# Performance work log

Hardware: AMD Instinct MI355X
Metric: run time of the kernel (lower is better)

Reference implementation:

```python
import jax, jax.numpy as jnp
import numpy as np

B, S, D, H = 2, 2048, 1024, 16
HD = D // H  # head dim 64
LN_EPS = 1e-12


def setup_inputs() -> dict:
    key = jax.random.key(0)
    ks = jax.random.split(key, 10)
    sc = 0.02
    return {
        "input_tensor": jax.random.normal(ks[0], (B, S, D), dtype=jnp.float32),
        "attention_mask": jnp.zeros((B, 1, 1, S), dtype=jnp.float32),
        "Wq": jax.random.normal(ks[1], (D, D), dtype=jnp.float32) * sc,
        "bq": jnp.zeros((D,), dtype=jnp.float32),
        "Wk": jax.random.normal(ks[2], (D, D), dtype=jnp.float32) * sc,
        "bk": jnp.zeros((D,), dtype=jnp.float32),
        "Wv": jax.random.normal(ks[3], (D, D), dtype=jnp.float32) * sc,
        "bv": jnp.zeros((D,), dtype=jnp.float32),
        "Wo": jax.random.normal(ks[4], (D, D), dtype=jnp.float32) * sc,
        "bo": jnp.zeros((D,), dtype=jnp.float32),
        "ln_gamma": jnp.ones((D,), dtype=jnp.float32),
        "ln_beta": jnp.zeros((D,), dtype=jnp.float32),
    }


def _split_heads(x):
    # [B,S,D] -> [B,H,S,hd]
    return x.reshape(B, S, H, HD).transpose(0, 2, 1, 3)


def reference(input_tensor, attention_mask, Wq, bq, Wk, bk, Wv, bv, Wo, bo, ln_gamma, ln_beta):
    q = _split_heads(input_tensor @ Wq + bq)
    k = _split_heads(input_tensor @ Wk + bk)
    v = _split_heads(input_tensor @ Wv + bv)
    scores = jnp.einsum("bhqd,bhkd->bhqk", q, k) / jnp.sqrt(jnp.float32(HD))
    scores = scores + attention_mask  # additive mask broadcast
    probs = jax.nn.softmax(scores, axis=-1)
    ctx = jnp.einsum("bhqk,bhkd->bhqd", probs, v)
    ctx = ctx.transpose(0, 2, 1, 3).reshape(B, S, D)
    hidden = ctx @ Wo + bo
    x = hidden + input_tensor
    mu = jnp.mean(x, axis=-1, keepdims=True)
    var = jnp.mean(jnp.square(x - mu), axis=-1, keepdims=True)
    return (x - mu) / jnp.sqrt(var + LN_EPS) * ln_gamma + ln_beta
```

## Files before the change

### kernel.cpp

```cpp
#include <hip/hip_runtime.h>
#include <stdint.h>

#define Bb 2
#define Ss 2048
#define Dd 1024
#define Hh 16
#define HD 64
#define Mtot 4096

typedef __bf16 bf16x8 __attribute__((ext_vector_type(8)));
typedef float f32x4 __attribute__((ext_vector_type(4)));
typedef float f32x16 __attribute__((ext_vector_type(16)));
typedef unsigned short ushort_t;

#if __has_builtin(__builtin_amdgcn_exp2f)
#define EXP2(x) __builtin_amdgcn_exp2f(x)
#else
#define EXP2(x) __expf((x) * 0.6931472f)
#endif

__device__ __forceinline__ float bf2f(ushort_t u) {
    union { uint32_t i; float f; } v;
    v.i = ((uint32_t)u) << 16;
    return v.f;
}

__device__ __forceinline__ ushort_t f2bf(float f) {
    union { float f; uint32_t i; } v;
    v.f = f;
    uint32_t u = v.i;
    u += 0x7FFFu + ((u >> 16) & 1u);
    return (ushort_t)(u >> 16);
}

__device__ __forceinline__ uint32_t cvtpk_bf16(float lo, float hi) {
    uint32_t r;
    asm("v_cvt_pk_bf16_f32 %0, %1, %2" : "=v"(r) : "v"(lo), "v"(hi));
    return r;
}

__device__ __forceinline__ float load_in(const void* p, size_t i, int isf32) {
    if (isf32) return ((const float*)p)[i];
    return bf2f(((const ushort_t*)p)[i]);
}

__device__ __forceinline__ void gload_lds16(const void* g, void* l) {
    __builtin_amdgcn_global_load_lds(
        (const __attribute__((address_space(1))) void*)g,
        (__attribute__((address_space(3))) void*)l, 16, 0, 0);
}

#define NVEC 525568ull
__global__ __launch_bounds__(256) void prep_k(
    const void* X, const void* mask, const void* bq, const void* bk,
    const void* bv, const void* bo, const void* g, const void* be,
    const void* Wq, const void* Wk, const void* Wv, const void* Wo,
    int* __restrict__ flag, ushort_t* __restrict__ cX,
    ushort_t* __restrict__ cMask, ushort_t* __restrict__ cB,
    ushort_t* __restrict__ wt) {
    __shared__ int sflag;
    __shared__ ushort_t tile[32][33];
    const int tid = threadIdx.x;
    {
        const int lane = tid & 63;
        if (tid < 64) {
            const ushort_t* Xu = (const ushort_t*)X;
            int local = 0;
            for (int i = lane; i < 2048; i += 64) {
                int e = (Xu[i] >> 7) & 0xFF;
                local += (e >= 0x90);
            }
            for (int off = 1; off < 64; off <<= 1) local += __shfl_xor(local, off);
            if (lane == 0) sflag = (local >= 4) ? 1 : 0;
        }
    }
    __syncthreads();
    const int f = sflag;
    if (blockIdx.x == 0 && tid == 0) *flag = f;

    if (blockIdx.x < 1024) {
        const size_t stride = 1024ull * 256ull;
        for (size_t t = (size_t)blockIdx.x * 256 + tid; t < NVEC; t += stride) {
            const void* src;
            ushort_t* dst;
            size_t v;
            if (t < 524288ull) {
                src = X; dst = cX; v = t;
            } else if (t < 524800ull) {
                src = mask; dst = cMask; v = t - 524288ull;
            } else {
                size_t j = t - 524800ull;
                int w = (int)(j >> 7);
                src = (w == 0) ? bq : (w == 1) ? bk : (w == 2) ? bv
                    : (w == 3) ? bo : (w == 4) ? g : be;
                dst = cB + w * 1024;
                v = j & 127;
            }
            if (f) {
                const float4* s4 = (const float4*)src;
                float4 a = s4[v * 2], b = s4[v * 2 + 1];
                union { ushort_t u[8]; uint4 q; } pk;
                pk.u[0] = f2bf(a.x); pk.u[1] = f2bf(a.y);
                pk.u[2] = f2bf(a.z); pk.u[3] = f2bf(a.w);
                pk.u[4] = f2bf(b.x); pk.u[5] = f2bf(b.y);
                pk.u[6] = f2bf(b.z); pk.u[7] = f2bf(b.w);
                ((uint4*)dst)[v] = pk.q;
            } else {
                ((uint4*)dst)[v] = ((const uint4*)src)[v];
            }
        }
    } else {
        int id2 = blockIdx.x - 1024;
        int z = id2 >> 10;
        int rem = id2 & 1023;
        int bx = rem & 31, by = rem >> 5;
        const void* W = (z == 0) ? Wq : (z == 1) ? Wk : (z == 2) ? Wv : Wo;
        ushort_t* T = wt + (size_t)z * Dd * Dd;
        int tx = tid & 31, ty = tid >> 5;
        int x = bx * 32 + tx;
        int y0 = by * 32;
        for (int i = 0; i < 4; i++) {
            int y = y0 + ty + i * 8;
            tile[ty + i * 8][tx] = f2bf(load_in(W, (size_t)y * Dd + x, f));
        }
        __syncthreads();
        int x2 = by * 32 + tx;
        int y20 = bx * 32;
        for (int i = 0; i < 4; i++) {
            int y = y20 + ty + i * 8;
            T[(size_t)y * Dd + x2] = tile[tx][ty + i * 8];
        }
    }
}

__global__ __launch_bounds__(256) void gemm_qkv(
    const ushort_t* __restrict__ X, const ushort_t* __restrict__ wt,
    const ushort_t* __restrict__ cB,
    ushort_t* __restrict__ Qb, ushort_t* __restrict__ Kb, ushort_t* __restrict__ Vtb) {
    const int z = blockIdx.z;
    const ushort_t* Wt = wt + (size_t)z * Dd * Dd;
    const ushort_t* bias = cB + z * 1024;

    __shared__ __align__(16) ushort_t smem[2][2][128 * 32];

    const int tid = threadIdx.x;
    const int lane = tid & 63, wv = tid >> 6;
    const int quad = lane >> 4, l15 = lane & 15;
    const int wrow = (wv >> 1) * 64, wcol = (wv & 1) * 64;
    const int row0 = blockIdx.y * 128, col0 = blockIdx.x * 128;
    const int lrow = lane >> 2, lcol = (lane & 3) * 8;

    const f32x4 fzero = {0.f, 0.f, 0.f, 0.f};
    f32x4 acc[4][4];
    for (int mt = 0; mt < 4; mt++)
        for (int nt = 0; nt < 4; nt++) acc[mt][nt] = fzero;

    for (int j = 0; j < 2; j++) {
        int ch = wv * 2 + j;
        gload_lds16(&X[(size_t)(row0 + ch * 16 + lrow) * Dd + lcol],
                    &smem[0][0][ch * 512]);
        gload_lds16(&Wt[(size_t)(col0 + ch * 16 + lrow) * Dd + lcol],
                    &smem[0][1][ch * 512]);
    }

    for (int k0 = 0; k0 < Dd; k0 += 32) {
        const int buf = (k0 >> 5) & 1;
        __syncthreads();
        if (k0 + 32 < Dd) {
            for (int j = 0; j < 2; j++) {
                int ch = wv * 2 + j;
                gload_lds16(&X[(size_t)(row0 + ch * 16 + lrow) * Dd + k0 + 32 + lcol],
                            &smem[buf ^ 1][0][ch * 512]);
                gload_lds16(&Wt[(size_t)(col0 + ch * 16 + lrow) * Dd + k0 + 32 + lcol],
                            &smem[buf ^ 1][1][ch * 512]);
            }
        }
        const ushort_t* As = &smem[buf][0][0];
        const ushort_t* Bs = &smem[buf][1][0];
        bf16x8 af[4], bfr[4];
        for (int mt = 0; mt < 4; mt++)
            af[mt] = *(const bf16x8*)(&As[(wrow + mt * 16 + l15) * 32 + quad * 8]);
        for (int nt = 0; nt < 4; nt++)
            bfr[nt] = *(const bf16x8*)(&Bs[(wcol + nt * 16 + l15) * 32 + quad * 8]);
        for (int mt = 0; mt < 4; mt++)
            for (int nt = 0; nt < 4; nt++)
                acc[mt][nt] = __builtin_amdgcn_mfma_f32_16x16x32_bf16(
                    af[mt], bfr[nt], acc[mt][nt], 0, 0, 0);
    }

    const float qscale = 0.18033688f;
    ushort_t* Cs = &smem[0][0][0];
    for (int mt = 0; mt < 4; mt++) {
        __syncthreads();
        for (int nt = 0; nt < 4; nt++) {
            int gn = col0 + wcol + nt * 16 + l15;
            float bv_ = bf2f(bias[gn]);
            for (int r = 0; r < 4; r++) {
                float v = acc[mt][nt][r] + bv_;
                if (z == 0) v *= qscale;
                int ric = (wv >> 1) * 16 + quad * 4 + r;
                Cs[ric * 136 + wcol + nt * 16 + l15] = f2bf(v);
            }
        }
        __syncthreads();
        if (z == 2) {
            int c = tid >> 1, r0 = (tid & 1) * 16;
            int gn = col0 + c, h = gn >> 6, d = gn & 63;
            int gmbase = row0 + (r0 >> 4) * 64 + mt * 16;
            int b = gmbase >> 11, s0 = gmbase & 2047;
            union { ushort_t u[16]; uint4 q[2]; } pk;
            for (int i = 0; i < 16; i++) pk.u[i] = Cs[(r0 + i) * 136 + c];
            uint4* dst = (uint4*)&Vtb[((size_t)((b * Hh + h) * HD + d)) * Ss + s0];
            dst[0] = pk.q[0];
            dst[1] = pk.q[1];
        } else {
            int ric = tid >> 3, c0 = (tid & 7) * 16;
            int gm = row0 + (ric >> 4) * 64 + mt * 16 + (ric & 15);
            int gn = col0 + c0, h = gn >> 6, d0 = gn & 63;
            int b = gm >> 11, s = gm & 2047;
            const uint4* src = (const uint4*)&Cs[ric * 136 + c0];
            ushort_t* Ob = (z == 0) ? Qb : Kb;
            uint4* dst = (uint4*)&Ob[((size_t)((b * Hh + h) * Ss + s)) * HD + d0];
            dst[0] = src[0];
            dst[1] = src[1];
        }
    }
}

__global__ __launch_bounds__(512, 4) void attn(
    const ushort_t* __restrict__ Q, const ushort_t* __restrict__ K,
    const ushort_t* __restrict__ Vt, const ushort_t* __restrict__ mask,
    ushort_t* __restrict__ ctx) {
    const int tid = threadIdx.x;
    const int lane = tid & 63, wv = tid >> 6;
    const int wg = wv & 3, g = wv >> 2;
    const int n = lane & 31, hi = lane >> 5;
    const int bh = blockIdx.x;
    const int b = bh >> 4, h = bh & 15;
    const int q0 = blockIdx.y * 128 + wg * 32;
    const int kg = g * 1024;

    const ushort_t* Qh = Q + (size_t)bh * Ss * HD;
    const ushort_t* Kh = K + (size_t)bh * Ss * HD;
    const ushort_t* Vh = Vt + (size_t)bh * HD * Ss;

    __shared__ __align__(16) ushort_t KV[2][2][2][64 * 64];
    __shared__ __align__(16) float maskF[Ss];

    for (int i = tid; i < Ss; i += 512)
        maskF[i] = (bf2f(mask[b * Ss + i]) - 4.0f) * 1.4426950f;

    const int r8 = lane >> 3, c8 = lane & 7, gc = c8 ^ r8;
    const int sw = n & 7;

    for (int j = 0; j < 2; j++) {
        int row = wg * 16 + j * 8;
        gload_lds16(&Kh[(size_t)(kg + row + r8) * HD + gc * 8], &KV[g][0][0][row * 64]);
        gload_lds16(&Vh[(size_t)(row + r8) * Ss + kg + gc * 8], &KV[g][1][0][row * 64]);
    }

    bf16x8 qf[4];
#pragma unroll
    for (int ks = 0; ks < 4; ks++)
        qf[ks] = *(const bf16x8*)(&Qh[(size_t)(q0 + n) * HD + ks * 16 + hi * 8]);

    bf16x8 onesf;
    {
        union { ushort_t u[8]; bf16x8 v; } ou;
        for (int i = 0; i < 8; i++) ou.u[i] = 0x3F80;
        onesf = ou.v;
    }

    f32x16 o[2], o_l;
#pragma unroll
    for (int r = 0; r < 16; r++) { o[0][r] = 0.f; o[1][r] = 0.f; o_l[r] = 0.f; }

    for (int it = 0; it < 16; it++) {
        const int kb = kg + it * 64;
        const int buf = it & 1;
        __syncthreads();

        if (it + 1 < 16) {
            for (int j = 0; j < 2; j++) {
                int row = wg * 16 + j * 8;
                gload_lds16(&Kh[(size_t)(kb + 64 + row + r8) * HD + gc * 8],
                            &KV[g][0][buf ^ 1][row * 64]);
                gload_lds16(&Vh[(size_t)(row + r8) * Ss + kb + 64 + gc * 8],
                            &KV[g][1][buf ^ 1][row * 64]);
            }
        }

        const ushort_t* ks_ = &KV[g][0][buf][0];
        const ushort_t* vs_ = &KV[g][1][buf][0];

        f32x16 st[2];
#pragma unroll
        for (int mt = 0; mt < 2; mt++) {
#pragma unroll
            for (int r4 = 0; r4 < 4; r4++) {
                f32x4 mk = *(const f32x4*)(&maskF[kb + mt * 32 + r4 * 8 + hi * 4]);
                st[mt][r4 * 4 + 0] = mk[0];
                st[mt][r4 * 4 + 1] = mk[1];
                st[mt][r4 * 4 + 2] = mk[2];
                st[mt][r4 * 4 + 3] = mk[3];
            }
        }
        __builtin_amdgcn_s_setprio(1);
#pragma unroll
        for (int mt = 0; mt < 2; mt++) {
#pragma unroll
            for (int ksp = 0; ksp < 4; ksp++) {
                bf16x8 kf = *(const bf16x8*)(
                    &ks_[(mt * 32 + n) * 64 + ((ksp * 2 + hi) ^ sw) * 8]);
                st[mt] = __builtin_amdgcn_mfma_f32_32x32x16_bf16(
                    kf, qf[ksp], st[mt], 0, 0, 0);
            }
        }
        __builtin_amdgcn_s_setprio(0);

#pragma unroll
        for (int mt = 0; mt < 2; mt++)
#pragma unroll
            for (int r = 0; r < 16; r++) st[mt][r] = EXP2(st[mt][r]);

#pragma unroll
        for (int c = 0; c < 4; c++) {
            const int mt = c >> 1, cc = (c & 1) * 8;
            uint32_t a0 = cvtpk_bf16(st[mt][cc + 0], st[mt][cc + 1]);
            uint32_t a1 = cvtpk_bf16(st[mt][cc + 2], st[mt][cc + 3]);
            uint32_t b0 = cvtpk_bf16(st[mt][cc + 4], st[mt][cc + 5]);
            uint32_t b1 = cvtpk_bf16(st[mt][cc + 6], st[mt][cc + 7]);
            asm("v_permlane32_swap_b32 %0, %1" : "+v"(a0), "+v"(b0));
            asm("v_permlane32_swap_b32 %0, %1" : "+v"(a1), "+v"(b1));
            union { uint32_t w[4]; bf16x8 v; } pa;
            pa.w[0] = a0; pa.w[1] = a1; pa.w[2] = b0; pa.w[3] = b1;
            __builtin_amdgcn_s_setprio(1);
#pragma unroll
            for (int dt = 0; dt < 2; dt++) {
                bf16x8 vf = *(const bf16x8*)(
                    &vs_[(dt * 32 + n) * 64 + ((c * 2 + hi) ^ sw) * 8]);
                o[dt] = __builtin_amdgcn_mfma_f32_32x32x16_bf16(
                    pa.v, vf, o[dt], 0, 0, 0);
            }
            o_l = __builtin_amdgcn_mfma_f32_32x32x16_bf16(
                pa.v, onesf, o_l, 0, 0, 0);
            __builtin_amdgcn_s_setprio(0);
        }
    }

    float* comb = (float*)&KV[0][0][0][0];
    float* combL = comb + 8192;
    __syncthreads();
    if (g == 1) {
#pragma unroll
        for (int r = 0; r < 16; r++) {
            combL[(wg * 16 + r) * 64 + lane] = o_l[r];
#pragma unroll
            for (int dt = 0; dt < 2; dt++)
                comb[((wg * 2 + dt) * 16 + r) * 64 + lane] = o[dt][r];
        }
    }
    __syncthreads();
    if (g == 0) {
#pragma unroll
        for (int r = 0; r < 16; r++) {
            int qa = q0 + (r & 3) + 8 * (r >> 2) + 4 * hi;
            float l = o_l[r] + combL[(wg * 16 + r) * 64 + lane];
            float linv = 1.f / l;
#pragma unroll
            for (int dt = 0; dt < 2; dt++) {
                float val = o[dt][r] + comb[((wg * 2 + dt) * 16 + r) * 64 + lane];
                ctx[((size_t)(b * Ss + qa)) * Dd + h * HD + dt * 32 + n] =
                    f2bf(val * linv);
            }
        }
    }
}

__global__ __launch_bounds__(256) void gemm_out(
    const ushort_t* __restrict__ A, const ushort_t* __restrict__ Wt,
    const ushort_t* __restrict__ bo, const ushort_t* __restrict__ X,
    ushort_t* __restrict__ xout) {
    __shared__ __align__(16) ushort_t smem[2][6144];

    const int tid = threadIdx.x;
    const int lane = tid & 63, wv = tid >> 6;
    const int quad = lane >> 4, l15 = lane & 15;
    const int wrow = (wv >> 1) * 32, wcol = (wv & 1) * 64;
    const int row0 = blockIdx.y * 64, col0 = blockIdx.x * 128;
    const int lrow = lane >> 2, lcol = (lane & 3) * 8;

    const f32x4 fzero = {0.f, 0.f, 0.f, 0.f};
    f32x4 acc[2][4];
    for (int mt = 0; mt < 2; mt++)
        for (int nt = 0; nt < 4; nt++) acc[mt][nt] = fzero;

    gload_lds16(&A[(size_t)(row0 + wv * 16 + lrow) * Dd + lcol], &smem[0][wv * 512]);
    for (int j = 0; j < 2; j++) {
        int ch = wv * 2 + j;
        gload_lds16(&Wt[(size_t)(col0 + ch * 16 + lrow) * Dd + lcol],
                    &smem[0][2048 + ch * 512]);
    }

    for (int k0 = 0; k0 < Dd; k0 += 32) {
        const int buf = (k0 >> 5) & 1;
        __syncthreads();
        if (k0 + 32 < Dd) {
            gload_lds16(&A[(size_t)(row0 + wv * 16 + lrow) * Dd + k0 + 32 + lcol],
                        &smem[buf ^ 1][wv * 512]);
            for (int j = 0; j < 2; j++) {
                int ch = wv * 2 + j;
                gload_lds16(&Wt[(size_t)(col0 + ch * 16 + lrow) * Dd + k0 + 32 + lcol],
                            &smem[buf ^ 1][2048 + ch * 512]);
            }
        }
        const ushort_t* As = &smem[buf][0];
        const ushort_t* Bs = &smem[buf][2048];
        bf16x8 af[2], bfr[4];
        for (int mt = 0; mt < 2; mt++)
            af[mt] = *(const bf16x8*)(&As[(wrow + mt * 16 + l15) * 32 + quad * 8]);
        for (int nt = 0; nt < 4; nt++)
            bfr[nt] = *(const bf16x8*)(&Bs[(wcol + nt * 16 + l15) * 32 + quad * 8]);
        for (int mt = 0; mt < 2; mt++)
            for (int nt = 0; nt < 4; nt++)
                acc[mt][nt] = __builtin_amdgcn_mfma_f32_16x16x32_bf16(
                    af[mt], bfr[nt], acc[mt][nt], 0, 0, 0);
    }

    for (int mt = 0; mt < 2; mt++)
        for (int nt = 0; nt < 4; nt++)
            for (int r = 0; r < 4; r++) {
                int gm = row0 + wrow + mt * 16 + quad * 4 + r;
                int gn = col0 + wcol + nt * 16 + l15;
                float v = acc[mt][nt][r] + bf2f(bo[gn]) + bf2f(X[(size_t)gm * Dd + gn]);
                xout[(size_t)gm * Dd + gn] = f2bf(v);
            }
}

__global__ __launch_bounds__(256) void ln_k(
    const ushort_t* __restrict__ x, const ushort_t* __restrict__ gamma,
    const ushort_t* __restrict__ beta, const int* __restrict__ flag,
    void* __restrict__ out) {
    const int row = blockIdx.x;
    const int tid = threadIdx.x;
    const int f = *flag;

    union { uint2 q; ushort_t u[4]; } xv;
    xv.q = ((const uint2*)(x + (size_t)row * Dd))[tid];
    float xi[4];
    for (int i = 0; i < 4; i++) xi[i] = bf2f(xv.u[i]);
    float s = (xi[0] + xi[1]) + (xi[2] + xi[3]);
    float ss = (xi[0] * xi[0] + xi[1] * xi[1]) + (xi[2] * xi[2] + xi[3] * xi[3]);
    for (int off = 1; off < 64; off <<= 1) {
        s += __shfl_xor(s, off);
        ss += __shfl_xor(ss, off);
    }
    __shared__ float ps[4], pss[4];
    int wv = tid >> 6;
    if ((tid & 63) == 0) { ps[wv] = s; pss[wv] = ss; }
    __syncthreads();
    s = ps[0] + ps[1] + ps[2] + ps[3];
    ss = pss[0] + pss[1] + pss[2] + pss[3];
    float mu = s * (1.f / Dd);
    float var = ss * (1.f / Dd) - mu * mu;
    float rstd = rsqrtf(fmaxf(var, 0.f) + 1e-12f);

    const int c0 = tid * 4;
    float r[4];
    for (int i = 0; i < 4; i++) {
        float g = bf2f(gamma[c0 + i]);
        float bb = bf2f(beta[c0 + i]);
        r[i] = (xi[i] - mu) * rstd * g + bb;
    }
    if (f) {
        float4 o4 = {r[0], r[1], r[2], r[3]};
        ((float4*)out)[(size_t)row * 256 + tid] = o4;
    } else {
        union { ushort_t u[4]; uint2 q; } pk;
        for (int i = 0; i < 4; i++) pk.u[i] = f2bf(r[i]);
        *(uint2*)((ushort_t*)out + (size_t)row * Dd + c0) = pk.q;
    }
}

extern "C" void kernel_launch(void* const* d_in, const int* in_sizes, int n_in,
                              void* d_out, int out_size, void* d_ws, size_t ws_size,
                              hipStream_t stream) {
    char* ws = (char*)d_ws;
    int* flag       = (int*)ws;
    ushort_t* cMask = (ushort_t*)(ws + (64ull << 10));
    ushort_t* cB    = (ushort_t*)(ws + (96ull << 10));
    ushort_t* cX    = (ushort_t*)(ws + (1ull << 20));
    ushort_t* wt    = (ushort_t*)(ws + (17ull << 20));
    ushort_t* Qb    = (ushort_t*)(ws + (25ull << 20));
    ushort_t* Kb    = (ushort_t*)(ws + (33ull << 20));
    ushort_t* Vtb   = (ushort_t*)(ws + (41ull << 20));
    ushort_t* ctx   = (ushort_t*)(ws + (49ull << 20));
    ushort_t* xbuf  = (ushort_t*)(ws + (25ull << 20));

    hipLaunchKernelGGL(prep_k, dim3(5120), dim3(256), 0, stream,
                       d_in[0], d_in[1], d_in[3], d_in[5], d_in[7], d_in[9],
                       d_in[10], d_in[11], d_in[2], d_in[4], d_in[6], d_in[8],
                       flag, cX, cMask, cB, wt);
    hipLaunchKernelGGL(gemm_qkv, dim3(8, 32, 3), dim3(256), 0, stream,
                       cX, wt, cB, Qb, Kb, Vtb);
    hipLaunchKernelGGL(attn, dim3(32, 16), dim3(512), 0, stream,
                       Qb, Kb, Vtb, cMask, ctx);
    hipLaunchKernelGGL(gemm_out, dim3(8, 64), dim3(256), 0, stream,
                       ctx, wt + 3ull * Dd * Dd, cB + 3 * 1024, cX, xbuf);
    hipLaunchKernelGGL(ln_k, dim3(Mtot), dim3(256), 0, stream,
                       xbuf, cB + 4 * 1024, cB + 5 * 1024, flag, d_out);
}
```

Baseline: 218.4 us.

## Process two query tiles per wave in attention to reuse K/V fragments

Each attention wave now handles 64 query rows (two 32-row tiles) instead of 32, so every K and V fragment read from LDS feeds two MFMAs. The grid is halved along the query axis and launch bounds drop to 2 blocks per CU to make room for the doubled accumulators. The cross-group combine is split into two phases to fit the scratch space. This cuts LDS traffic and global K/V reloads per query, at the cost of much higher register pressure, lower occupancy, and fewer blocks (256), which may underfill the GPU.

```diff
diff --git a/kernel.cpp b/kernel.cpp
--- a/kernel.cpp
+++ b/kernel.cpp
@@ -227,7 +227,7 @@
     }
 }
 
-__global__ __launch_bounds__(512, 4) void attn(
+__global__ __launch_bounds__(512, 2) void attn(
     const ushort_t* __restrict__ Q, const ushort_t* __restrict__ K,
     const ushort_t* __restrict__ Vt, const ushort_t* __restrict__ mask,
     ushort_t* __restrict__ ctx) {
@@ -237,7 +237,7 @@
     const int n = lane & 31, hi = lane >> 5;
     const int bh = blockIdx.x;
     const int b = bh >> 4, h = bh & 15;
-    const int q0 = blockIdx.y * 128 + wg * 32;
+    const int q0 = blockIdx.y * 256 + wg * 64;
     const int kg = g * 1024;
 
     const ushort_t* Qh = Q + (size_t)bh * Ss * HD;
@@ -259,10 +259,12 @@
         gload_lds16(&Vh[(size_t)(row + r8) * Ss + kg + gc * 8], &KV[g][1][0][row * 64]);
     }
 
-    bf16x8 qf[4];
-#pragma unroll
-    for (int ks = 0; ks < 4; ks++)
-        qf[ks] = *(const bf16x8*)(&Qh[(size_t)(q0 + n) * HD + ks * 16 + hi * 8]);
+    bf16x8 qfX[4], qfY[4];
+#pragma unroll
+    for (int ks = 0; ks < 4; ks++) {
+        qfX[ks] = *(const bf16x8*)(&Qh[(size_t)(q0 + n) * HD + ks * 16 + hi * 8]);
+        qfY[ks] = *(const bf16x8*)(&Qh[(size_t)(q0 + 32 + n) * HD + ks * 16 + hi * 8]);
+    }
 
     bf16x8 onesf;
     {
@@ -271,9 +273,12 @@
         onesf = ou.v;
     }
 
-    f32x16 o[2], o_l;
-#pragma unroll
-    for (int r = 0; r < 16; r++) { o[0][r] = 0.f; o[1][r] = 0.f; o_l[r] = 0.f; }
+    f32x16 oX[2], oY[2], olX, olY;
+#pragma unroll
+    for (int r = 0; r < 16; r++) {
+        oX[0][r] = 0.f; oX[1][r] = 0.f; oY[0][r] = 0.f; oY[1][r] = 0.f;
+        olX[r] = 0.f; olY[r] = 0.f;
+    }
 
     for (int it = 0; it < 16; it++) {
         const int kb = kg + it * 64;
@@ -293,16 +298,17 @@
         const ushort_t* ks_ = &KV[g][0][buf][0];
         const ushort_t* vs_ = &KV[g][1][buf][0];
 
-        f32x16 st[2];
+        f32x16 stX[2], stY[2];
 #pragma unroll
         for (int mt = 0; mt < 2; mt++) {
 #pragma unroll
             for (int r4 = 0; r4 < 4; r4++) {
                 f32x4 mk = *(const f32x4*)(&maskF[kb + mt * 32 + r4 * 8 + hi * 4]);
-                st[mt][r4 * 4 + 0] = mk[0];
-                st[mt][r4 * 4 + 1] = mk[1];
-                st[mt][r4 * 4 + 2] = mk[2];
-                st[mt][r4 * 4 + 3] = mk[3];
+#pragma unroll
+                for (int j = 0; j < 4; j++) {
+                    stX[mt][r4 * 4 + j] = mk[j];
+                    stY[mt][r4 * 4 + j] = mk[j];
+                }
             }
         }
         __builtin_amdgcn_s_setprio(1);
@@ -312,8 +318,10 @@
             for (int ksp = 0; ksp < 4; ksp++) {
                 bf16x8 kf = *(const bf16x8*)(
                     &ks_[(mt * 32 + n) * 64 + ((ksp * 2 + hi) ^ sw) * 8]);
-                st[mt] = __builtin_amdgcn_mfma_f32_32x32x16_bf16(
-                    kf, qf[ksp], st[mt], 0, 0, 0);
+                stX[mt] = __builtin_amdgcn_mfma_f32_32x32x16_bf16(
+                    kf, qfX[ksp], stX[mt], 0, 0, 0);
+                stY[mt] = __builtin_amdgcn_mfma_f32_32x32x16_bf16(
+                    kf, qfY[ksp], stY[mt], 0, 0, 0);
             }
         }
         __builtin_amdgcn_s_setprio(0);
@@ -321,43 +329,61 @@
 #pragma unroll
         for (int mt = 0; mt < 2; mt++)
 #pragma unroll
-            for (int r = 0; r < 16; r++) st[mt][r] = EXP2(st[mt][r]);
+            for (int r = 0; r < 16; r++) {
+                stX[mt][r] = EXP2(stX[mt][r]);
+                stY[mt][r] = EXP2(stY[mt][r]);
+            }
 
 #pragma unroll
         for (int c = 0; c < 4; c++) {
             const int mt = c >> 1, cc = (c & 1) * 8;
-            uint32_t a0 = cvtpk_bf16(st[mt][cc + 0], st[mt][cc + 1]);
-            uint32_t a1 = cvtpk_bf16(st[mt][cc + 2], st[mt][cc + 3]);
-            uint32_t b0 = cvtpk_bf16(st[mt][cc + 4], st[mt][cc + 5]);
-            uint32_t b1 = cvtpk_bf16(st[mt][cc + 6], st[mt][cc + 7]);
-            asm("v_permlane32_swap_b32 %0, %1" : "+v"(a0), "+v"(b0));
-            asm("v_permlane32_swap_b32 %0, %1" : "+v"(a1), "+v"(b1));
-            union { uint32_t w[4]; bf16x8 v; } pa;
-            pa.w[0] = a0; pa.w[1] = a1; pa.w[2] = b0; pa.w[3] = b1;
+            uint32_t a0X = cvtpk_bf16(stX[mt][cc + 0], stX[mt][cc + 1]);
+            uint32_t a1X = cvtpk_bf16(stX[mt][cc + 2], stX[mt][cc + 3]);
+            uint32_t b0X = cvtpk_bf16(stX[mt][cc + 4], stX[mt][cc + 5]);
+            uint32_t b1X = cvtpk_bf16(stX[mt][cc + 6], stX[mt][cc + 7]);
+            asm("v_permlane32_swap_b32 %0, %1" : "+v"(a0X), "+v"(b0X));
+            asm("v_permlane32_swap_b32 %0, %1" : "+v"(a1X), "+v"(b1X));
+            union { uint32_t w[4]; bf16x8 v; } paX;
+            paX.w[0] = a0X; paX.w[1] = a1X; paX.w[2] = b0X; paX.w[3] = b1X;
+
+            uint32_t a0Y = cvtpk_bf16(stY[mt][cc + 0], stY[mt][cc + 1]);
+            uint32_t a1Y = cvtpk_bf16(stY[mt][cc + 2], stY[mt][cc + 3]);
+            uint32_t b0Y = cvtpk_bf16(stY[mt][cc + 4], stY[mt][cc + 5]);
+            uint32_t b1Y = cvtpk_bf16(stY[mt][cc + 6], stY[mt][cc + 7]);
+            asm("v_permlane32_swap_b32 %0, %1" : "+v"(a0Y), "+v"(b0Y));
+            asm("v_permlane32_swap_b32 %0, %1" : "+v"(a1Y), "+v"(b1Y));
+            union { uint32_t w[4]; bf16x8 v; } paY;
+            paY.w[0] = a0Y; paY.w[1] = a1Y; paY.w[2] = b0Y; paY.w[3] = b1Y;
+
             __builtin_amdgcn_s_setprio(1);
 #pragma unroll
             for (int dt = 0; dt < 2; dt++) {
                 bf16x8 vf = *(const bf16x8*)(
                     &vs_[(dt * 32 + n) * 64 + ((c * 2 + hi) ^ sw) * 8]);
-                o[dt] = __builtin_amdgcn_mfma_f32_32x32x16_bf16(
-                    pa.v, vf, o[dt], 0, 0, 0);
-            }
-            o_l = __builtin_amdgcn_mfma_f32_32x32x16_bf16(
-                pa.v, onesf, o_l, 0, 0, 0);
+                oX[dt] = __builtin_amdgcn_mfma_f32_32x32x16_bf16(
+                    paX.v, vf, oX[dt], 0, 0, 0);
+                oY[dt] = __builtin_amdgcn_mfma_f32_32x32x16_bf16(
+                    paY.v, vf, oY[dt], 0, 0, 0);
+            }
+            olX = __builtin_amdgcn_mfma_f32_32x32x16_bf16(
+                paX.v, onesf, olX, 0, 0, 0);
+            olY = __builtin_amdgcn_mfma_f32_32x32x16_bf16(
+                paY.v, onesf, olY, 0, 0, 0);
             __builtin_amdgcn_s_setprio(0);
         }
     }
 
-    float* comb = (float*)&KV[0][0][0][0];
-    float* combL = comb + 8192;
+    float* scrO = (float*)&KV[0][0][0][0];
+    float* scrL = (float*)&KV[1][0][0][0];
     __syncthreads();
     if (g == 1) {
 #pragma unroll
         for (int r = 0; r < 16; r++) {
-            combL[(wg * 16 + r) * 64 + lane] = o_l[r];
+            scrL[(wg * 32 + r) * 64 + lane] = olX[r];
+            scrL[(wg * 32 + 16 + r) * 64 + lane] = olY[r];
 #pragma unroll
             for (int dt = 0; dt < 2; dt++)
-                comb[((wg * 2 + dt) * 16 + r) * 64 + lane] = o[dt][r];
+                scrO[(wg * 32 + dt * 16 + r) * 64 + lane] = oX[dt][r];
         }
     }
     __syncthreads();
@@ -365,11 +391,34 @@
 #pragma unroll
         for (int r = 0; r < 16; r++) {
             int qa = q0 + (r & 3) + 8 * (r >> 2) + 4 * hi;
-            float l = o_l[r] + combL[(wg * 16 + r) * 64 + lane];
+            float l = olX[r] + scrL[(wg * 32 + r) * 64 + lane];
             float linv = 1.f / l;
 #pragma unroll
             for (int dt = 0; dt < 2; dt++) {
-                float val = o[dt][r] + comb[((wg * 2 + dt) * 16 + r) * 64 + lane];
+                float val = oX[dt][r] + scrO[(wg * 32 + dt * 16 + r) * 64 + lane];
+                ctx[((size_t)(b * Ss + qa)) * Dd + h * HD + dt * 32 + n] =
+                    f2bf(val * linv);
+            }
+        }
+    }
+    __syncthreads();
+    if (g == 1) {
+#pragma unroll
+        for (int r = 0; r < 16; r++)
+#pragma unroll
+            for (int dt = 0; dt < 2; dt++)
+                scrO[(wg * 32 + dt * 16 + r) * 64 + lane] = oY[dt][r];
+    }
+    __syncthreads();
+    if (g == 0) {
+#pragma unroll
+        for (int r = 0; r < 16; r++) {
+            int qa = q0 + 32 + (r & 3) + 8 * (r >> 2) + 4 * hi;
+            float l = olY[r] + scrL[(wg * 32 + 16 + r) * 64 + lane];
+            float linv = 1.f / l;
+#pragma unroll
+            for (int dt = 0; dt < 2; dt++) {
+                float val = oY[dt][r] + scrO[(wg * 32 + dt * 16 + r) * 64 + lane];
                 ctx[((size_t)(b * Ss + qa)) * Dd + h * HD + dt * 32 + n] =
                     f2bf(val * linv);
             }
@@ -503,7 +552,7 @@
                        flag, cX, cMask, cB, wt);
     hipLaunchKernelGGL(gemm_qkv, dim3(8, 32, 3), dim3(256), 0, stream,
                        cX, wt, cB, Qb, Kb, Vtb);
-    hipLaunchKernelGGL(attn, dim3(32, 16), dim3(512), 0, stream,
+    hipLaunchKernelGGL(attn, dim3(32, 8), dim3(512), 0, stream,
                        Qb, Kb, Vtb, cMask, ctx);
     hipLaunchKernelGGL(gemm_out, dim3(8, 64), dim3(256), 0, stream,
                        ctx, wt + 3ull * Dd * Dd, cB + 3 * 1024, cX, xbuf);
```

New measurement: 206.1 us. 5.6% less time.
